# Kernel optimization log

Measured on AMD Instinct MI355X. Metric: run time of the kernel, lower is better.

## Reference

```python
import jax, jax.numpy as jnp
import numpy as np

K = 1024
D = 64
BETA = 0.25


def setup_inputs() -> dict:
    key = jax.random.key(0)
    k1, k2 = jax.random.split(key)
    x = jax.random.normal(k1, (32, D, 64, 64), dtype=jnp.float32)
    # torch init: uniform(-1/K, 1/K)
    emb = jax.random.uniform(k2, (K, D), dtype=jnp.float32, minval=-1.0 / K, maxval=1.0 / K)
    return {"x": x, "emb": emb}


def reference(x, emb):
    B, C, H, W = x.shape
    z = jnp.transpose(x, (0, 2, 3, 1))          # [B,H,W,D]
    zf = z.reshape(-1, C)                        # [N,D]
    # squared euclidean distances ||z||^2 + ||e||^2 - 2 z.e
    dist = (jnp.sum(zf * zf, axis=1, keepdims=True)
            + jnp.sum(emb * emb, axis=1)
            - 2.0 * jnp.matmul(zf, emb.T))       # [N,K]
    min_idx = jnp.argmin(dist, axis=1)           # [N]
    # one-hot @ emb == gather
    z_q = emb[min_idx].reshape(z.shape)          # [B,H,W,D]
    sg = jax.lax.stop_gradient
    embedding_loss = (jnp.mean((sg(z_q) - z) ** 2)
                      + BETA * jnp.mean((z_q - sg(z)) ** 2))
    z_q_st = z + sg(z_q - z)                     # straight-through
    # code-usage perplexity
    n = zf.shape[0]
    e_mean = jnp.bincount(min_idx, length=K).astype(z.dtype) / n
    perplexity = jnp.exp(-jnp.sum(e_mean * jnp.log(e_mean + 1e-10)))
    z_q_out = jnp.transpose(z_q_st, (0, 3, 1, 2))  # [B,D,H,W]
    return embedding_loss, z_q_out, perplexity
```

## Files before the change

### kernel.cpp

```cpp
#include <hip/hip_runtime.h>
#include <math.h>

#define D_    64
#define K_    1024
#define N_    131072
#define HW_   4096
#define TAU   2e-5f

typedef unsigned long long ull;
typedef unsigned short ushort;
typedef short  bf16x8  __attribute__((ext_vector_type(8)));
typedef float  f32x4   __attribute__((ext_vector_type(4)));
typedef ushort ushort8 __attribute__((ext_vector_type(8)));

__device__ __forceinline__ ushort f2bf(float f) {
    unsigned u = __float_as_uint(f);
    return (ushort)((u + 0x7FFFu + ((u >> 16) & 1u)) >> 16);
}
__device__ __forceinline__ float b2f(ushort h) {
    return __uint_as_float((unsigned)h << 16);
}

__global__ __launch_bounds__(256)
void vq_prep(const float* __restrict__ x, const float* __restrict__ emb,
             float* __restrict__ r2g, ushort* __restrict__ ehg,
             ushort* __restrict__ elg, float* __restrict__ e2g,
             float* __restrict__ embT, int* __restrict__ hist,
             int* __restrict__ cnt, double* __restrict__ ssqd) {
    const int n = blockIdx.x * 256 + threadIdx.x;
    const int b = n >> 12, hw = n & (HW_ - 1);
    const float* xr = x + (size_t)b * (D_ * HW_) + hw;
    float r2 = 0.0f;
    #pragma unroll
    for (int d = 0; d < D_; ++d) { float z = xr[(size_t)d * HW_]; r2 = fmaf(z, z, r2); }
    r2g[n] = r2;

    if (n < K_) {
        const float* er = emb + (size_t)n * D_;
        float e2 = 0.0f;
        #pragma unroll
        for (int d8 = 0; d8 < 8; ++d8) {
            ushort8 hh, ll;
            #pragma unroll
            for (int j = 0; j < 8; ++j) {
                float e = er[d8 * 8 + j];
                e2 = fmaf(e, e, e2);
                ushort h = f2bf(e);
                hh[j] = h;
                ll[j] = f2bf(e - b2f(h));
                embT[(size_t)(d8 * 8 + j) * K_ + n] = e;
            }
            *(ushort8*)(ehg + (size_t)n * D_ + d8 * 8) = hh;
            *(ushort8*)(elg + (size_t)n * D_ + d8 * 8) = ll;
        }
        e2g[n] = e2;
        hist[n] = 0;
    }
    if (n == 0) { *cnt = 0; *ssqd = 0.0; }
}

#define LOADB(KT, BH0, BH1, BL0, BL1, E2)                                     \
    {                                                                         \
        int c_ = (KT) * 16 + c16;                                             \
        const ushort* eb_ = ehg + (size_t)c_ * D_ + g * 8;                    \
        BH0 = *(const bf16x8*)(eb_);                                          \
        BH1 = *(const bf16x8*)(eb_ + 32);                                     \
        const ushort* lb_ = elg + (size_t)c_ * D_ + g * 8;                    \
        BL0 = *(const bf16x8*)(lb_);                                          \
        BL1 = *(const bf16x8*)(lb_ + 32);                                     \
        E2 = e2g[c_];                                                         \
    }

#define COMPUTE(KT, BH0, BH1, BL0, BL1, E2)                                   \
    {                                                                         \
        const int c_ = (KT) * 16 + c16;                                       \
        f32x4 ac[4];                                                          \
        _Pragma("unroll")                                                     \
        for (int t = 0; t < 4; ++t) {                                         \
            f32x4 a = {0.0f, 0.0f, 0.0f, 0.0f};                               \
            a = __builtin_amdgcn_mfma_f32_16x16x32_bf16(ah[t][0], BH0, a, 0, 0, 0); \
            a = __builtin_amdgcn_mfma_f32_16x16x32_bf16(al[t][0], BH0, a, 0, 0, 0); \
            a = __builtin_amdgcn_mfma_f32_16x16x32_bf16(ah[t][1], BH1, a, 0, 0, 0); \
            a = __builtin_amdgcn_mfma_f32_16x16x32_bf16(al[t][1], BH1, a, 0, 0, 0); \
            a = __builtin_amdgcn_mfma_f32_16x16x32_bf16(ah[t][0], BL0, a, 0, 0, 0); \
            a = __builtin_amdgcn_mfma_f32_16x16x32_bf16(ah[t][1], BL1, a, 0, 0, 0); \
            ac[t] = a;                                                        \
        }                                                                     \
        _Pragma("unroll")                                                     \
        for (int t = 0; t < 4; ++t) {                                         \
            _Pragma("unroll")                                                 \
            for (int q = 0; q < 4; ++q) {                                     \
                float dist = fmaf(-2.0f, ac[t][q], r2v[t * 4 + q] + E2);      \
                const int st = t * 4 + q;                                     \
                bool lt = dist < v1[st];                                      \
                v2[st] = lt ? v1[st] : fminf(v2[st], dist);                   \
                k1[st] = lt ? c_ : k1[st];                                    \
                v1[st] = lt ? dist : v1[st];                                  \
            }                                                                 \
        }                                                                     \
    }

__global__ __launch_bounds__(256)
void vq_mfma(const float* __restrict__ x, const ushort* __restrict__ ehg,
             const ushort* __restrict__ elg, const float* __restrict__ e2g,
             const float* __restrict__ r2g, int* __restrict__ bidx,
             int* __restrict__ list, int* __restrict__ cnt,
             int* __restrict__ hist) {
    const int tid = threadIdx.x;
    const int wv  = tid >> 6;
    const int l   = tid & 63;
    const int g   = l >> 4;
    const int c16 = l & 15;
    const int n0w = blockIdx.x * 256 + wv * 64;

    bf16x8 ah[4][2], al[4][2];
    #pragma unroll
    for (int t = 0; t < 4; ++t) {
        const int row = n0w + t * 16 + c16;
        const int b = row >> 12, hw = row & (HW_ - 1);
        const float* xr = x + (size_t)b * (D_ * HW_) + hw;
        #pragma unroll
        for (int s = 0; s < 2; ++s) {
            #pragma unroll
            for (int j = 0; j < 8; ++j) {
                float z = xr[(size_t)(g * 8 + s * 32 + j) * HW_];
                ushort h = f2bf(z);
                ah[t][s][j] = (short)h;
                al[t][s][j] = (short)f2bf(z - b2f(h));
            }
        }
    }

    float r2v[16];
    #pragma unroll
    for (int t = 0; t < 4; ++t)
        #pragma unroll
        for (int q = 0; q < 4; ++q)
            r2v[t * 4 + q] = r2g[n0w + t * 16 + 4 * g + q];

    float v1[16], v2[16]; int k1[16];
    #pragma unroll
    for (int st = 0; st < 16; ++st) { v1[st] = 3.4e38f; v2[st] = 3.4e38f; k1[st] = 0; }

    bf16x8 pbh0, pbh1, pbl0, pbl1; float pe2;
    LOADB(0, pbh0, pbh1, pbl0, pbl1, pe2)
    for (int kt = 0; kt < 64; kt += 2) {
        bf16x8 qbh0, qbh1, qbl0, qbl1; float qe2;
        LOADB(kt + 1, qbh0, qbh1, qbl0, qbl1, qe2)
        COMPUTE(kt, pbh0, pbh1, pbl0, pbl1, pe2)
        const int ktn = (kt + 2 < 64) ? kt + 2 : 63;
        LOADB(ktn, pbh0, pbh1, pbl0, pbl1, pe2)
        COMPUTE(kt + 1, qbh0, qbh1, qbl0, qbl1, qe2)
    }

    #pragma unroll
    for (int off = 1; off < 16; off <<= 1) {
        #pragma unroll
        for (int st = 0; st < 16; ++st) {
            float w1 = __shfl_xor(v1[st], off, 64);
            float w2 = __shfl_xor(v2[st], off, 64);
            int   wk = __shfl_xor(k1[st], off, 64);
            float lose = (w1 < v1[st]) ? v1[st] : w1;
            v2[st] = fminf(fminf(v2[st], w2), lose);
            if (w1 < v1[st]) { v1[st] = w1; k1[st] = wk; }
        }
    }

    if (c16 == 0) {
        #pragma unroll
        for (int t = 0; t < 4; ++t) {
            #pragma unroll
            for (int q = 0; q < 4; ++q) {
                const int st = t * 4 + q;
                const int n = n0w + t * 16 + 4 * g + q;
                if (!(v2[st] - v1[st] > TAU)) {
                    int i = atomicAdd(cnt, 1);
                    list[i] = n;
                } else {
                    bidx[n] = k1[st];
                    atomicAdd(&hist[k1[st]], 1);
                }
            }
        }
    }
}

__global__ __launch_bounds__(256)
void vq_exact(const float* __restrict__ x, const float* __restrict__ embT,
              const float* __restrict__ e2g, const float* __restrict__ r2g,
              const int* __restrict__ list, const int* __restrict__ cnt,
              int* __restrict__ bidx, int* __restrict__ hist) {
    const int l  = threadIdx.x & 63;
    const int gw = (blockIdx.x * 256 + threadIdx.x) >> 6;
    const int nw = (gridDim.x * 256) >> 6;
    const int C  = *cnt;
    for (int i = gw; i < C; i += nw) {
        const int n = list[i];
        const int b = n >> 12, hw = n & (HW_ - 1);
        const float* xr = x + (size_t)b * (D_ * HW_) + hw;
        const float zval = xr[(size_t)l * HW_];
        const float r2 = r2g[n];
        float s[16];
        #pragma unroll
        for (int j = 0; j < 16; ++j) s[j] = 0.0f;
        for (int d = 0; d < D_; ++d) {
            const float zd = __shfl(zval, d, 64);
            const float* erow = embT + (size_t)d * K_ + l * 4;
            const float4 e0 = *(const float4*)(erow);
            const float4 e1 = *(const float4*)(erow + 256);
            const float4 e2 = *(const float4*)(erow + 512);
            const float4 e3 = *(const float4*)(erow + 768);
            s[0]  = fmaf(zd, e0.x, s[0]);  s[1]  = fmaf(zd, e0.y, s[1]);
            s[2]  = fmaf(zd, e0.z, s[2]);  s[3]  = fmaf(zd, e0.w, s[3]);
            s[4]  = fmaf(zd, e1.x, s[4]);  s[5]  = fmaf(zd, e1.y, s[5]);
            s[6]  = fmaf(zd, e1.z, s[6]);  s[7]  = fmaf(zd, e1.w, s[7]);
            s[8]  = fmaf(zd, e2.x, s[8]);  s[9]  = fmaf(zd, e2.y, s[9]);
            s[10] = fmaf(zd, e2.z, s[10]); s[11] = fmaf(zd, e2.w, s[11]);
            s[12] = fmaf(zd, e3.x, s[12]); s[13] = fmaf(zd, e3.y, s[13]);
            s[14] = fmaf(zd, e3.z, s[14]); s[15] = fmaf(zd, e3.w, s[15]);
        }
        ull best = ~0ull;
        #pragma unroll
        for (int j = 0; j < 16; ++j) {
            const int k = (j >> 2) * 256 + l * 4 + (j & 3);
            float dist = fmaf(-2.0f, s[j], r2 + e2g[k]);
            ull p = ((ull)__float_as_uint(dist) << 32) | (unsigned)k;
            if (p < best) best = p;
        }
        #pragma unroll
        for (int off = 1; off < 64; off <<= 1) {
            ull q = __shfl_xor(best, off, 64);
            if (q < best) best = q;
        }
        if (l == 0) {
            int k = (int)(best & 0xffffffffull);
            bidx[n] = k;
            atomicAdd(&hist[k], 1);
        }
    }
}

__global__ __launch_bounds__(256)
void vq_apply(const float* __restrict__ x, const float* __restrict__ emb,
              const int* __restrict__ bidx, float* __restrict__ zq_out,
              double* __restrict__ ssqd) {
    const int row = blockIdx.x * 256 + threadIdx.x;
    const int b = row >> 12, hw = row & (HW_ - 1);
    const float* xr   = x      + (size_t)b * (D_ * HW_) + hw;
    float*       outr = zq_out + (size_t)b * (D_ * HW_) + hw;
    const int k = bidx[row];
    const float* er = emb + (size_t)k * D_;
    float ls = 0.0f;
    #pragma unroll
    for (int d = 0; d < D_; ++d) {
        float zv = xr[(size_t)d * HW_];
        float t  = er[d] - zv;
        ls = fmaf(t, t, ls);
        outr[(size_t)d * HW_] = zv + t;
    }
    #pragma unroll
    for (int o = 32; o > 0; o >>= 1) ls += __shfl_down(ls, o, 64);
    if ((threadIdx.x & 63) == 0) atomicAdd(ssqd, (double)ls);
}

__global__ __launch_bounds__(1024)
void vq_final(const int* __restrict__ hist, const double* __restrict__ ssqd,
              float* __restrict__ out_loss, float* __restrict__ out_perp) {
    __shared__ float wred[16];
    int t = threadIdx.x;
    float cnt = (float)hist[t];
    float em  = cnt / (float)N_;
    float s   = em * logf(em + 1e-10f);
    #pragma unroll
    for (int o = 32; o > 0; o >>= 1) s += __shfl_down(s, o, 64);
    if ((t & 63) == 0) wred[t >> 6] = s;
    __syncthreads();
    if (t == 0) {
        float tot = 0.0f;
        for (int w = 0; w < 16; ++w) tot += wred[w];
        *out_perp = expf(-tot);
        float mse = (float)(*ssqd / (double)((size_t)N_ * D_));
        *out_loss = mse + 0.25f * mse;
    }
}

extern "C" void kernel_launch(void* const* d_in, const int* in_sizes, int n_in,
                              void* d_out, int out_size, void* d_ws, size_t ws_size,
                              hipStream_t stream) {
    const float* x   = (const float*)d_in[0];
    const float* emb = (const float*)d_in[1];
    float* out  = (float*)d_out;
    float* loss = out;
    float* zq   = out + 1;
    float* perp = out + 1 + (size_t)N_ * D_;

    char* w = (char*)d_ws;
    float*  r2g  = (float*)w;   w += (size_t)N_ * 4;
    int*    bidx = (int*)w;     w += (size_t)N_ * 4;
    int*    list = (int*)w;     w += (size_t)N_ * 4;
    ushort* ehg  = (ushort*)w;  w += (size_t)K_ * D_ * 2;
    ushort* elg  = (ushort*)w;  w += (size_t)K_ * D_ * 2;
    float*  embT = (float*)w;   w += (size_t)K_ * D_ * 4;
    float*  e2g  = (float*)w;   w += (size_t)K_ * 4;
    int*    hist = (int*)w;     w += (size_t)K_ * 4;
    int*    cnt  = (int*)w;     w += 16;
    double* ssqd = (double*)w;

    vq_prep<<<dim3(N_ / 256), dim3(256), 0, stream>>>(x, emb, r2g, ehg, elg, e2g, embT, hist, cnt, ssqd);
    vq_mfma<<<dim3(N_ / 256), dim3(256), 0, stream>>>(x, ehg, elg, e2g, r2g, bidx, list, cnt, hist);
    vq_exact<<<dim3(2048), dim3(256), 0, stream>>>(x, embT, e2g, r2g, list, cnt, bidx, hist);
    vq_apply<<<dim3(N_ / 256), dim3(256), 0, stream>>>(x, emb, bidx, zq, ssqd);
    vq_final<<<dim3(1), dim3(1024), 0, stream>>>(hist, ssqd, loss, perp);
}
```

Before: 179.6 us.

## Drop per-row norm from argmin, shrink MFMA wave tile, recompute norm in exact pass

```diff
diff --git a/kernel.cpp b/kernel.cpp
--- a/kernel.cpp
+++ b/kernel.cpp
@@ -5,7 +5,7 @@
 #define K_    1024
 #define N_    131072
 #define HW_   4096
-#define TAU   2e-5f
+#define TAU   4e-5f
 
 typedef unsigned long long ull;
 typedef unsigned short ushort;
@@ -22,19 +22,11 @@
 }
 
 __global__ __launch_bounds__(256)
-void vq_prep(const float* __restrict__ x, const float* __restrict__ emb,
-             float* __restrict__ r2g, ushort* __restrict__ ehg,
+void vq_prep(const float* __restrict__ emb, ushort* __restrict__ ehg,
              ushort* __restrict__ elg, float* __restrict__ e2g,
              float* __restrict__ embT, int* __restrict__ hist,
              int* __restrict__ cnt, double* __restrict__ ssqd) {
     const int n = blockIdx.x * 256 + threadIdx.x;
-    const int b = n >> 12, hw = n & (HW_ - 1);
-    const float* xr = x + (size_t)b * (D_ * HW_) + hw;
-    float r2 = 0.0f;
-    #pragma unroll
-    for (int d = 0; d < D_; ++d) { float z = xr[(size_t)d * HW_]; r2 = fmaf(z, z, r2); }
-    r2g[n] = r2;
-
     if (n < K_) {
         const float* er = emb + (size_t)n * D_;
         float e2 = 0.0f;
@@ -56,7 +48,7 @@
         e2g[n] = e2;
         hist[n] = 0;
     }
-    if (n == 0) { *cnt = 0; *ssqd = 0.0; }
+    if (n == 0 && blockIdx.x == 0) { *cnt = 0; *ssqd = 0.0; }
 }
 
 #define LOADB(KT, BH0, BH1, BL0, BL1, E2)                                     \
@@ -74,9 +66,9 @@
 #define COMPUTE(KT, BH0, BH1, BL0, BL1, E2)                                   \
     {                                                                         \
         const int c_ = (KT) * 16 + c16;                                       \
-        f32x4 ac[4];                                                          \
+        f32x4 ac[2];                                                          \
         _Pragma("unroll")                                                     \
-        for (int t = 0; t < 4; ++t) {                                         \
+        for (int t = 0; t < 2; ++t) {                                         \
             f32x4 a = {0.0f, 0.0f, 0.0f, 0.0f};                               \
             a = __builtin_amdgcn_mfma_f32_16x16x32_bf16(ah[t][0], BH0, a, 0, 0, 0); \
             a = __builtin_amdgcn_mfma_f32_16x16x32_bf16(al[t][0], BH0, a, 0, 0, 0); \
@@ -87,10 +79,10 @@
             ac[t] = a;                                                        \
         }                                                                     \
         _Pragma("unroll")                                                     \
-        for (int t = 0; t < 4; ++t) {                                         \
+        for (int t = 0; t < 2; ++t) {                                         \
             _Pragma("unroll")                                                 \
             for (int q = 0; q < 4; ++q) {                                     \
-                float dist = fmaf(-2.0f, ac[t][q], r2v[t * 4 + q] + E2);      \
+                float dist = fmaf(-2.0f, ac[t][q], E2);                       \
                 const int st = t * 4 + q;                                     \
                 bool lt = dist < v1[st];                                      \
                 v2[st] = lt ? v1[st] : fminf(v2[st], dist);                   \
@@ -103,19 +95,18 @@
 __global__ __launch_bounds__(256)
 void vq_mfma(const float* __restrict__ x, const ushort* __restrict__ ehg,
              const ushort* __restrict__ elg, const float* __restrict__ e2g,
-             const float* __restrict__ r2g, int* __restrict__ bidx,
-             int* __restrict__ list, int* __restrict__ cnt,
-             int* __restrict__ hist) {
+             int* __restrict__ bidx, int* __restrict__ list,
+             int* __restrict__ cnt, int* __restrict__ hist) {
     const int tid = threadIdx.x;
     const int wv  = tid >> 6;
     const int l   = tid & 63;
     const int g   = l >> 4;
     const int c16 = l & 15;
-    const int n0w = blockIdx.x * 256 + wv * 64;
-
-    bf16x8 ah[4][2], al[4][2];
-    #pragma unroll
-    for (int t = 0; t < 4; ++t) {
+    const int n0w = blockIdx.x * 128 + wv * 32;
+
+    bf16x8 ah[2][2], al[2][2];
+    #pragma unroll
+    for (int t = 0; t < 2; ++t) {
         const int row = n0w + t * 16 + c16;
         const int b = row >> 12, hw = row & (HW_ - 1);
         const float* xr = x + (size_t)b * (D_ * HW_) + hw;
@@ -131,16 +122,9 @@
         }
     }
 
-    float r2v[16];
-    #pragma unroll
-    for (int t = 0; t < 4; ++t)
-        #pragma unroll
-        for (int q = 0; q < 4; ++q)
-            r2v[t * 4 + q] = r2g[n0w + t * 16 + 4 * g + q];
-
-    float v1[16], v2[16]; int k1[16];
-    #pragma unroll
-    for (int st = 0; st < 16; ++st) { v1[st] = 3.4e38f; v2[st] = 3.4e38f; k1[st] = 0; }
+    float v1[8], v2[8]; int k1[8];
+    #pragma unroll
+    for (int st = 0; st < 8; ++st) { v1[st] = 3.4e38f; v2[st] = 3.4e38f; k1[st] = 0; }
 
     bf16x8 pbh0, pbh1, pbl0, pbl1; float pe2;
     LOADB(0, pbh0, pbh1, pbl0, pbl1, pe2)
@@ -156,7 +140,7 @@
     #pragma unroll
     for (int off = 1; off < 16; off <<= 1) {
         #pragma unroll
-        for (int st = 0; st < 16; ++st) {
+        for (int st = 0; st < 8; ++st) {
             float w1 = __shfl_xor(v1[st], off, 64);
             float w2 = __shfl_xor(v2[st], off, 64);
             int   wk = __shfl_xor(k1[st], off, 64);
@@ -168,7 +152,7 @@
 
     if (c16 == 0) {
         #pragma unroll
-        for (int t = 0; t < 4; ++t) {
+        for (int t = 0; t < 2; ++t) {
             #pragma unroll
             for (int q = 0; q < 4; ++q) {
                 const int st = t * 4 + q;
@@ -187,9 +171,9 @@
 
 __global__ __launch_bounds__(256)
 void vq_exact(const float* __restrict__ x, const float* __restrict__ embT,
-              const float* __restrict__ e2g, const float* __restrict__ r2g,
-              const int* __restrict__ list, const int* __restrict__ cnt,
-              int* __restrict__ bidx, int* __restrict__ hist) {
+              const float* __restrict__ e2g, const int* __restrict__ list,
+              const int* __restrict__ cnt, int* __restrict__ bidx,
+              int* __restrict__ hist) {
     const int l  = threadIdx.x & 63;
     const int gw = (blockIdx.x * 256 + threadIdx.x) >> 6;
     const int nw = (gridDim.x * 256) >> 6;
@@ -199,12 +183,13 @@
         const int b = n >> 12, hw = n & (HW_ - 1);
         const float* xr = x + (size_t)b * (D_ * HW_) + hw;
         const float zval = xr[(size_t)l * HW_];
-        const float r2 = r2g[n];
+        float r2 = 0.0f;
         float s[16];
         #pragma unroll
         for (int j = 0; j < 16; ++j) s[j] = 0.0f;
         for (int d = 0; d < D_; ++d) {
             const float zd = __shfl(zval, d, 64);
+            r2 = fmaf(zd, zd, r2);
             const float* erow = embT + (size_t)d * K_ + l * 4;
             const float4 e0 = *(const float4*)(erow);
             const float4 e1 = *(const float4*)(erow + 256);
@@ -295,7 +280,6 @@
     float* perp = out + 1 + (size_t)N_ * D_;
 
     char* w = (char*)d_ws;
-    float*  r2g  = (float*)w;   w += (size_t)N_ * 4;
     int*    bidx = (int*)w;     w += (size_t)N_ * 4;
     int*    list = (int*)w;     w += (size_t)N_ * 4;
     ushort* ehg  = (ushort*)w;  w += (size_t)K_ * D_ * 2;
@@ -306,9 +290,9 @@
     int*    cnt  = (int*)w;     w += 16;
     double* ssqd = (double*)w;
 
-    vq_prep<<<dim3(N_ / 256), dim3(256), 0, stream>>>(x, emb, r2g, ehg, elg, e2g, embT, hist, cnt, ssqd);
-    vq_mfma<<<dim3(N_ / 256), dim3(256), 0, stream>>>(x, ehg, elg, e2g, r2g, bidx, list, cnt, hist);
-    vq_exact<<<dim3(2048), dim3(256), 0, stream>>>(x, embT, e2g, r2g, list, cnt, bidx, hist);
+    vq_prep<<<dim3(4), dim3(256), 0, stream>>>(emb, ehg, elg, e2g, embT, hist, cnt, ssqd);
+    vq_mfma<<<dim3(N_ / 128), dim3(256), 0, stream>>>(x, ehg, elg, e2g, bidx, list, cnt, hist);
+    vq_exact<<<dim3(2048), dim3(256), 0, stream>>>(x, embT, e2g, list, cnt, bidx, hist);
     vq_apply<<<dim3(N_ / 256), dim3(256), 0, stream>>>(x, emb, bidx, zq, ssqd);
     vq_final<<<dim3(1), dim3(1024), 0, stream>>>(hist, ssqd, loss, perp);
 }
```

New measurement: 223.3 us. +24.3%, slower.
